# Optimization experiments

Measured on AMD Instinct MI355X. Metric: run time of the kernel, lower is better.

The kernel has to match this reference:

```python
import jax, jax.numpy as jnp
from jax import lax
import numpy as np

B, T, IN = 256, 128, 64
H = 1024            # unified hidden size (encoder fc/lstm == decoder lstm, required by the code)
QW, QL = 128, 128
V = QW * QL         # decoder_output_size_fc
K, DELTA = 5, 16


def _lin(x, w, b):
    return x @ w.T + b


def _lstm(x, h0, c0, wih, whh, bih, bhh):
    # x: [B,T,I]; h0,c0: [B,H]. PyTorch gate order: i, f, g, o.
    xg = jnp.einsum('bti,gi->btg', x, wih) + bih  # precompute input projections [B,T,4H]
    def step(carry, xt):
        h, c = carry
        g = xt + h @ whh.T + bhh
        i, f, gg, o = jnp.split(g, 4, axis=-1)
        c = jax.nn.sigmoid(f) * c + jax.nn.sigmoid(i) * jnp.tanh(gg)
        h = jax.nn.sigmoid(o) * jnp.tanh(c)
        return (h, c), h
    (h, c), ys = lax.scan(step, (h0, c0), jnp.swapaxes(xg, 0, 1))
    return jnp.swapaxes(ys, 0, 1), h, c


def setup_inputs() -> dict:
    key = jax.random.key(0)
    ks = iter(jax.random.split(key, 64))
    def u(shape, fan):
        s = 1.0 / np.sqrt(fan)
        return jax.random.uniform(next(ks), shape, jnp.float32, -s, s)
    def lin_p(o, i):
        return u((o, i), i), u((o,), i)
    def lstm_p(i, h):
        return u((4 * h, i), h), u((4 * h, h), h), u((4 * h,), h), u((4 * h,), h)
    d = {'x': jax.random.normal(next(ks), (B, T, IN), jnp.float32)}
    d['efc1_w'], d['efc1_b'] = lin_p(H, IN)
    d['efc2_w'], d['efc2_b'] = lin_p(H, H)
    d['efc3_w'], d['efc3_b'] = lin_p(H, H)
    d['el1_wih'], d['el1_whh'], d['el1_bih'], d['el1_bhh'] = lstm_p(H, H)
    d['el2_wih'], d['el2_whh'], d['el2_bih'], d['el2_bhh'] = lstm_p(H, H)
    d['dl1_wih'], d['dl1_whh'], d['dl1_bih'], d['dl1_bhh'] = lstm_p(H, H)
    d['dl2_wih'], d['dl2_whh'], d['dl2_bih'], d['dl2_bhh'] = lstm_p(H, H)
    d['dfc1_w'], d['dfc1_b'] = lin_p(H, H)
    d['dfc2_w'], d['dfc2_b'] = lin_p(H, H)
    d['dfc3_w'], d['dfc3_b'] = lin_p(V, H)
    d['fqw_w'], d['fqw_b'] = lin_p(H // 2, QW)
    d['fql_w'], d['fql_b'] = lin_p(H // 2, QL)
    return d


def _forward(x, efc1_w, efc1_b, efc2_w, efc2_b, efc3_w, efc3_b,
             el1_wih, el1_whh, el1_bih, el1_bhh, el2_wih, el2_whh, el2_bih, el2_bhh,
             dl1_wih, dl1_whh, dl1_bih, dl1_bhh, dl2_wih, dl2_whh, dl2_bih, dl2_bhh,
             dfc1_w, dfc1_b, dfc2_w, dfc2_b, dfc3_w, dfc3_b,
             fqw_w, fqw_b, fql_w, fql_b):
    b = x.shape[0]
    # ---- encoder: 3 plain linears (no activation, as in source), then two stacked LSTMs ----
    e = _lin(_lin(_lin(x, efc1_w, efc1_b), efc2_w, efc2_b), efc3_w, efc3_b)
    z = jnp.zeros((b, H), x.dtype)
    e, h1, c1 = _lstm(e, z, z, el1_wih, el1_whh, el1_bih, el1_bhh)
    e, h2, c2 = _lstm(e, z, z, el2_wih, el2_whh, el2_bih, el2_bhh)  # lstm2 gets fresh zero state, as in source
    xs = e[:, -1:, :]  # last timestep [B,1,H]

    def once(xs, h1, c1, h2, c2):
        xs, h1, c1 = _lstm(xs, h1, c1, dl1_wih, dl1_whh, dl1_bih, dl1_bhh)
        xs, h2, c2 = _lstm(xs, h2, c2, dl2_wih, dl2_whh, dl2_bih, dl2_bhh)
        xs = _lin(_lin(_lin(xs, dfc1_w, dfc1_b), dfc2_w, dfc2_b), dfc3_w, dfc3_b)
        return xs, h1, c1, h2, c2

    def beam(scores, kcur, decoded, step):
        # scores: [B,V]; top-k == torch.sort(descending)[:, :kcur]
        _, idx = lax.top_k(scores, kcur)
        fw = idx // QL  # find_w
        fl = idx % QL   # find_l
        iw = jax.nn.one_hot(fw, QW, dtype=scores.dtype)  # [B,kcur,QW]
        il = jax.nn.one_hot(fl, QL, dtype=scores.dtype)  # [B,kcur,QL]
        decoded = decoded.at[:, step, :kcur, 0].set(fl.astype(decoded.dtype))
        decoded = decoded.at[:, step, :kcur, 1].set(fw.astype(decoded.dtype))
        return iw, il, decoded

    out, h1, c1, h2, c2 = once(xs, h1, c1, h2, c2)
    decoded = jnp.zeros((b, DELTA, K, 2), jnp.float32)
    iw, il, decoded = beam(out[:, 0, :], K, decoded, 0)
    iw = _lin(iw, fqw_w, fqw_b)  # [B,K,H/2]
    il = _lin(il, fql_w, fql_b)
    # source sets decoder_K = 1 after the first step: only beam slot 0 is ever expanded
    for t in range(DELTA - 1):
        emb = jnp.concatenate([iw[:, 0, :], il[:, 0, :]], axis=-1)[:, None, :]  # [B,1,H]
        out, h1, c1, h2, c2 = once(emb, h1, c1, h2, c2)
        iw, il, decoded = beam(out[:, 0, :], 1, decoded, t + 1)
        iw = _lin(iw, fqw_w, fqw_b)
        il = _lin(il, fql_w, fql_b)
    return decoded


def reference(x, efc1_w, efc1_b, efc2_w, efc2_b, efc3_w, efc3_b,
              el1_wih, el1_whh, el1_bih, el1_bhh, el2_wih, el2_whh, el2_bih, el2_bhh,
              dl1_wih, dl1_whh, dl1_bih, dl1_bhh, dl2_wih, dl2_whh, dl2_bih, dl2_bhh,
              dfc1_w, dfc1_b, dfc2_w, dfc2_b, dfc3_w, dfc3_b,
              fqw_w, fqw_b, fql_w, fql_b):
    return _forward(x, efc1_w, efc1_b, efc2_w, efc2_b, efc3_w, efc3_b,
                    el1_wih, el1_whh, el1_bih, el1_bhh, el2_wih, el2_whh, el2_bih, el2_bhh,
                    dl1_wih, dl1_whh, dl1_bih, dl1_bhh, dl2_wih, dl2_whh, dl2_bih, dl2_bhh,
                    dfc1_w, dfc1_b, dfc2_w, dfc2_b, dfc3_w, dfc3_b,
                    fqw_w, fqw_b, fql_w, fql_b)
```

## Files before the change

### kernel.cpp

```cpp
#include <hip/hip_runtime.h>
#include <math.h>

#define Hn     1024
#define Bn     256
#define Tn     128
#define Vn     16384
#define DELTAn 16
#define Kn     5
#define QLn    128

typedef _Float16 h8 __attribute__((ext_vector_type(8)));
typedef _Float16 h4 __attribute__((ext_vector_type(4)));
typedef float    f32x4 __attribute__((ext_vector_type(4)));

#define MFMA16(a, b, c) __builtin_amdgcn_mfma_f32_16x16x32_f16(a, b, c, 0, 0, 0)

#define WFRAG_4096 8388608

__global__ __launch_bounds__(256) void wconv_frag(
    const float* __restrict__ W, _Float16* __restrict__ wf, int ngb)
{
    int wid  = (blockIdx.x * 256 + threadIdx.x) >> 6;
    int lane = threadIdx.x & 63;
    int gb = wid >> 5, ks = wid & 31;
    if (gb >= ngb) return;
    const float* src = W + (size_t)(gb * 16 + (lane & 15)) * 1024 + ks * 32 + (lane >> 4) * 8;
    float4 v0 = *(const float4*)src;
    float4 v1 = *(const float4*)(src + 4);
    float vv[8] = {v0.x, v0.y, v0.z, v0.w, v1.x, v1.y, v1.z, v1.w};
    h8 vh, vl;
    #pragma unroll
    for (int j = 0; j < 8; ++j) {
        _Float16 hh = (_Float16)vv[j];
        vh[j] = hh;
        vl[j] = (_Float16)(vv[j] - (float)hh);
    }
    _Float16* dst = wf + ((size_t)(gb * 32 + ks) * 2) * 512 + lane * 8;
    *(h8*)dst        = vh;
    *(h8*)(dst + 512) = vl;
}

__global__ __launch_bounds__(256) void gemm_nt_128(
    const float* __restrict__ A, int lda, const float* __restrict__ W, int K,
    const float* __restrict__ bias, _Float16* __restrict__ yhi,
    _Float16* __restrict__ ylo, int ldy)
{
    __shared__ float As[16 * 132];
    __shared__ float Bs[16 * 132];
    const int bm   = blockIdx.y << 7;
    const int bn   = blockIdx.x << 7;
    const int tid  = threadIdx.x;
    const int tx   = (tid & 15) << 3;
    const int ty   = (tid >> 4) << 3;
    const int lrow = tid >> 1;
    const int lk   = (tid & 1) << 3;

    float acc[8][8] = {};
    const float* arow = A + (size_t)(bm + lrow) * lda + lk;
    const float* brow = W + (size_t)(bn + lrow) * K   + lk;

    for (int kt = 0; kt < K; kt += 16) {
        float4 a0 = *(const float4*)(arow + kt);
        float4 a1 = *(const float4*)(arow + kt + 4);
        float4 b0 = *(const float4*)(brow + kt);
        float4 b1 = *(const float4*)(brow + kt + 4);
        __syncthreads();
        As[(lk + 0) * 132 + lrow] = a0.x; As[(lk + 1) * 132 + lrow] = a0.y;
        As[(lk + 2) * 132 + lrow] = a0.z; As[(lk + 3) * 132 + lrow] = a0.w;
        As[(lk + 4) * 132 + lrow] = a1.x; As[(lk + 5) * 132 + lrow] = a1.y;
        As[(lk + 6) * 132 + lrow] = a1.z; As[(lk + 7) * 132 + lrow] = a1.w;
        Bs[(lk + 0) * 132 + lrow] = b0.x; Bs[(lk + 1) * 132 + lrow] = b0.y;
        Bs[(lk + 2) * 132 + lrow] = b0.z; Bs[(lk + 3) * 132 + lrow] = b0.w;
        Bs[(lk + 4) * 132 + lrow] = b1.x; Bs[(lk + 5) * 132 + lrow] = b1.y;
        Bs[(lk + 6) * 132 + lrow] = b1.z; Bs[(lk + 7) * 132 + lrow] = b1.w;
        __syncthreads();
        #pragma unroll
        for (int k = 0; k < 16; ++k) {
            float4 x0 = *(const float4*)(As + k * 132 + ty);
            float4 x1 = *(const float4*)(As + k * 132 + ty + 4);
            float4 y0 = *(const float4*)(Bs + k * 132 + tx);
            float4 y1 = *(const float4*)(Bs + k * 132 + tx + 4);
            float av[8] = {x0.x, x0.y, x0.z, x0.w, x1.x, x1.y, x1.z, x1.w};
            float bv[8] = {y0.x, y0.y, y0.z, y0.w, y1.x, y1.y, y1.z, y1.w};
            #pragma unroll
            for (int i = 0; i < 8; ++i)
                #pragma unroll
                for (int j = 0; j < 8; ++j)
                    acc[i][j] += av[i] * bv[j];
        }
    }

    #pragma unroll
    for (int i = 0; i < 8; ++i) {
        h8 vh, vl;
        #pragma unroll
        for (int j = 0; j < 8; ++j) {
            float v = acc[i][j] + bias[bn + tx + j];
            _Float16 hh = (_Float16)v;
            vh[j] = hh;
            vl[j] = (_Float16)(v - (float)hh);
        }
        size_t ro = (size_t)(bm + ty + i) * ldy + bn + tx;
        *(h8*)(yhi + ro) = vh;
        *(h8*)(ylo + ro) = vl;
    }
}

__global__ __launch_bounds__(256) void gemm_mfma4(
    const _Float16* __restrict__ Ahi, const _Float16* __restrict__ Alo, long long lda,
    const _Float16* __restrict__ wf, const float* __restrict__ bias,
    float* __restrict__ Y, long long ldy,
    _Float16* __restrict__ yhi, _Float16* __restrict__ ylo, int log2mt)
{
    __shared__ _Float16 lds[2][256 * 40];
    const int lin  = blockIdx.x;
    const int bt   = (lin >> 3) & ((1 << log2mt) - 1);
    const int nt   = (lin & 7) | ((lin >> (3 + log2mt)) << 3);
    const int bn   = nt << 6;
    const int bmB  = bt << 8;
    const int tid  = threadIdx.x;
    const int lane = tid & 63, wv = tid >> 6;
    const int l15  = lane & 15, quad = lane >> 4;
    const int r    = tid;

    f32x4 acc[4][4];
    #pragma unroll
    for (int mi = 0; mi < 4; ++mi)
        #pragma unroll
        for (int nf = 0; nf < 4; ++nf) acc[mi][nf] = (f32x4){0.f, 0.f, 0.f, 0.f};

    h8 ph[4], pl[4];
    h8 BhA[4], BlA[4], BhB[4], BlB[4];
    {
        size_t off = (size_t)(bmB + r) * lda;
        #pragma unroll
        for (int j = 0; j < 4; ++j) {
            ph[j] = *(const h8*)(Ahi + off + j * 8);
            pl[j] = *(const h8*)(Alo + off + j * 8);
        }
        #pragma unroll
        for (int nf = 0; nf < 4; ++nf) {
            const _Float16* bp = wf + ((size_t)(((nt << 2) + nf) * 32) * 2) * 512 + lane * 8;
            BhA[nf] = *(const h8*)bp;
            BlA[nf] = *(const h8*)(bp + 512);
        }
    }

#define G4_SI(SI, BHU, BLU, BHF, BLF)                                          \
    {                                                                          \
        __syncthreads();                                                       \
        _Pragma("unroll")                                                      \
        for (int j = 0; j < 4; ++j) {                                          \
            *(h8*)(&lds[0][r * 40 + j * 8]) = ph[j];                           \
            *(h8*)(&lds[1][r * 40 + j * 8]) = pl[j];                           \
        }                                                                      \
        __syncthreads();                                                       \
        {                                                                      \
            int sn = ((SI) + 1 < 32) ? (SI) + 1 : (SI);                        \
            size_t off = (size_t)(bmB + r) * lda + (sn << 5);                  \
            _Pragma("unroll")                                                  \
            for (int j = 0; j < 4; ++j) {                                      \
                ph[j] = *(const h8*)(Ahi + off + j * 8);                       \
                pl[j] = *(const h8*)(Alo + off + j * 8);                       \
            }                                                                  \
            _Pragma("unroll")                                                  \
            for (int nf = 0; nf < 4; ++nf) {                                   \
                const _Float16* bp = wf +                                      \
                    ((size_t)(((nt << 2) + nf) * 32 + sn) * 2) * 512 + lane * 8;\
                BHF[nf] = *(const h8*)bp;                                      \
                BLF[nf] = *(const h8*)(bp + 512);                              \
            }                                                                  \
        }                                                                      \
        h8 axh[4], axl[4];                                                     \
        _Pragma("unroll")                                                      \
        for (int mi = 0; mi < 4; ++mi) {                                       \
            int row = (wv << 6) + (mi << 4) + l15;                             \
            axh[mi] = *(const h8*)(&lds[0][row * 40 + quad * 8]);              \
            axl[mi] = *(const h8*)(&lds[1][row * 40 + quad * 8]);              \
        }                                                                      \
        _Pragma("unroll")                                                      \
        for (int nf = 0; nf < 4; ++nf)                                         \
            _Pragma("unroll")                                                  \
            for (int mi = 0; mi < 4; ++mi) {                                   \
                acc[mi][nf] = MFMA16(axh[mi], BHU[nf], acc[mi][nf]);           \
                acc[mi][nf] = MFMA16(axh[mi], BLU[nf], acc[mi][nf]);           \
                acc[mi][nf] = MFMA16(axl[mi], BHU[nf], acc[mi][nf]);           \
            }                                                                  \
    }

    for (int si = 0; si < 32; si += 2) {
        G4_SI(si,     BhA, BlA, BhB, BlB);
        G4_SI(si + 1, BhB, BlB, BhA, BlA);
    }
#undef G4_SI

    #pragma unroll
    for (int nf = 0; nf < 4; ++nf) {
        int col = bn + nf * 16 + l15;
        float bv = bias[col];
        #pragma unroll
        for (int mi = 0; mi < 4; ++mi) {
            #pragma unroll
            for (int rr = 0; rr < 4; ++rr) {
                int m = bmB + (wv << 6) + (mi << 4) + (quad << 2) + rr;
                float v = acc[mi][nf][rr] + bv;
                size_t ro = (size_t)m * ldy + col;
                if (yhi) {
                    _Float16 hh = (_Float16)v;
                    yhi[ro] = hh;
                    ylo[ro] = (_Float16)(v - (float)hh);
                } else {
                    Y[ro] = v;
                }
            }
        }
    }
}

__global__ __launch_bounds__(256, 2) void gemm_mfma_s(
    const _Float16* __restrict__ Ahi, const _Float16* __restrict__ Alo, long long lda,
    const _Float16* __restrict__ wf, const float* __restrict__ bias,
    _Float16* __restrict__ yhi, _Float16* __restrict__ ylo, long long ldy)
{
    __shared__ _Float16 lds[2][64 * 40];
    const int bn   = blockIdx.x << 6;
    const int bm   = blockIdx.y << 6;
    const int tid  = threadIdx.x;
    const int lane = tid & 63, wv = tid >> 6;
    const int l15  = lane & 15, quad = lane >> 4;
    const int r    = tid >> 2, kq = (tid & 3) << 3;

    f32x4 acc[4];
    #pragma unroll
    for (int nf = 0; nf < 4; ++nf) acc[nf] = (f32x4){0.f, 0.f, 0.f, 0.f};

    h8 pAh, pAl;
    h8 BhA[4], BlA[4], BhB[4], BlB[4];
    {
        size_t off = (size_t)(bm + r) * lda + kq;
        pAh = *(const h8*)(Ahi + off);
        pAl = *(const h8*)(Alo + off);
        #pragma unroll
        for (int nf = 0; nf < 4; ++nf) {
            const _Float16* bp = wf + ((size_t)(((bn >> 4) + nf) * 32) * 2) * 512 + lane * 8;
            BhA[nf] = *(const h8*)bp;
            BlA[nf] = *(const h8*)(bp + 512);
        }
    }

#define GS_SI(SI, BHU, BLU, BHF, BLF)                                          \
    {                                                                          \
        __syncthreads();                                                       \
        *(h8*)(&lds[0][r * 40 + kq]) = pAh;                                    \
        *(h8*)(&lds[1][r * 40 + kq]) = pAl;                                    \
        __syncthreads();                                                       \
        {                                                                      \
            int sn = ((SI) + 1 < 32) ? (SI) + 1 : (SI);                        \
            size_t off = (size_t)(bm + r) * lda + (sn << 5) + kq;              \
            pAh = *(const h8*)(Ahi + off);                                     \
            pAl = *(const h8*)(Alo + off);                                     \
            _Pragma("unroll")                                                  \
            for (int nf = 0; nf < 4; ++nf) {                                   \
                const _Float16* bp = wf +                                      \
                    ((size_t)(((bn >> 4) + nf) * 32 + sn) * 2) * 512 + lane * 8;\
                BHF[nf] = *(const h8*)bp;                                      \
                BLF[nf] = *(const h8*)(bp + 512);                              \
            }                                                                  \
        }                                                                      \
        int row = (wv << 4) + l15;                                             \
        h8 axh = *(const h8*)(&lds[0][row * 40 + quad * 8]);                   \
        h8 axl = *(const h8*)(&lds[1][row * 40 + quad * 8]);                   \
        _Pragma("unroll")                                                      \
        for (int nf = 0; nf < 4; ++nf) {                                       \
            acc[nf] = MFMA16(axh, BHU[nf], acc[nf]);                           \
            acc[nf] = MFMA16(axh, BLU[nf], acc[nf]);                           \
            acc[nf] = MFMA16(axl, BHU[nf], acc[nf]);                           \
        }                                                                      \
    }

    for (int si = 0; si < 32; si += 2) {
        GS_SI(si,     BhA, BlA, BhB, BlB);
        GS_SI(si + 1, BhB, BlB, BhA, BlA);
    }
#undef GS_SI

    #pragma unroll
    for (int nf = 0; nf < 4; ++nf) {
        int col = bn + nf * 16 + l15;
        float bv = bias[col];
        #pragma unroll
        for (int rr = 0; rr < 4; ++rr) {
            int m = bm + (wv << 4) + (quad << 2) + rr;
            float v = acc[nf][rr] + bv;
            size_t ro = (size_t)m * ldy + col;
            _Float16 hh = (_Float16)v;
            yhi[ro] = hh;
            ylo[ro] = (_Float16)(v - (float)hh);
        }
    }
}

struct LstmSet {
    const _Float16 *xhi, *xlo; long long ldx;
    const _Float16 *hphi, *hplo;
    const _Float16 *wf;
    const float *bih, *bhh;
    float *c;
    _Float16 *hohi, *holo;
};

__global__ __launch_bounds__(256, 2) void lstm_mfma4(LstmSet s0, LstmSet s1)
{
    const int lin = blockIdx.x;
    const int bt  = (lin >> 3) & 3;
    const int jz  = (lin & 7) | ((lin >> 5) << 3);
    const int jt  = jz & 63;
    LstmSet s = (jz >> 6) ? s1 : s0;
    if (s.wf == nullptr) return;
    __shared__ _Float16 lds[2][64 * 72];
    const int tid  = threadIdx.x;
    const int bm   = bt << 6;
    const int lane = tid & 63, wv = tid >> 6;
    const int l15  = lane & 15, quad = lane >> 4;
    const int r    = tid >> 2, kq = (tid & 3) << 4;

    f32x4 acc[4];
    #pragma unroll
    for (int nf = 0; nf < 4; ++nf) acc[nf] = (f32x4){0.f, 0.f, 0.f, 0.f};

    h8 pA[4];
    h8 BhA[8], BlA[8], BhB[8], BlB[8];
    {
        size_t off = (size_t)(bm + r) * s.ldx + kq;
        pA[0] = *(const h8*)(s.xhi + off); pA[1] = *(const h8*)(s.xhi + off + 8);
        pA[2] = *(const h8*)(s.xlo + off); pA[3] = *(const h8*)(s.xlo + off + 8);
        #pragma unroll
        for (int sub = 0; sub < 2; ++sub)
            #pragma unroll
            for (int nf = 0; nf < 4; ++nf) {
                const _Float16* bp = s.wf +
                    ((size_t)((nf * 64 + jt) * 32 + sub) * 2) * 512 + lane * 8;
                BhA[sub * 4 + nf] = *(const h8*)bp;
                BlA[sub * 4 + nf] = *(const h8*)(bp + 512);
            }
    }

#define LS_SI(SI, BHU, BLU, BHF, BLF)                                          \
    {                                                                          \
        __syncthreads();                                                       \
        *(h8*)(&lds[0][r * 72 + kq])     = pA[0];                              \
        *(h8*)(&lds[0][r * 72 + kq + 8]) = pA[1];                              \
        *(h8*)(&lds[1][r * 72 + kq])     = pA[2];                              \
        *(h8*)(&lds[1][r * 72 + kq + 8]) = pA[3];                              \
        __syncthreads();                                                       \
        {                                                                      \
            int sn  = ((SI) + 1 < 32) ? (SI) + 1 : (SI);                       \
            int phx = sn >> 4;                                                 \
            const _Float16* xh = phx ? s.hphi : s.xhi;                         \
            const _Float16* xl = phx ? s.hplo : s.xlo;                         \
            long long ld = phx ? Hn : s.ldx;                                   \
            size_t off = (size_t)(bm + r) * ld + ((sn & 15) << 6) + kq;        \
            pA[0] = *(const h8*)(xh + off); pA[1] = *(const h8*)(xh + off + 8);\
            pA[2] = *(const h8*)(xl + off); pA[3] = *(const h8*)(xl + off + 8);\
            const _Float16* wb = s.wf + (size_t)(sn >> 4) * WFRAG_4096;        \
            int ksb = (sn & 15) << 1;                                          \
            _Pragma("unroll")                                                  \
            for (int sub = 0; sub < 2; ++sub)                                  \
                _Pragma("unroll")                                              \
                for (int nf = 0; nf < 4; ++nf) {                               \
                    const _Float16* bp = wb +                                  \
                        ((size_t)((nf * 64 + jt) * 32 + ksb + sub) * 2) * 512  \
                        + lane * 8;                                            \
                    BHF[sub * 4 + nf] = *(const h8*)bp;                        \
                    BLF[sub * 4 + nf] = *(const h8*)(bp + 512);                \
                }                                                              \
        }                                                                      \
        const _Float16* wbc = s.wf + (size_t)((SI) >> 4) * WFRAG_4096;         \
        (void)wbc;                                                             \
        _Pragma("unroll")                                                      \
        for (int sub = 0; sub < 2; ++sub) {                                    \
            int row = (wv << 4) + l15;                                         \
            h8 axh = *(const h8*)(&lds[0][row * 72 + sub * 32 + quad * 8]);    \
            h8 axl = *(const h8*)(&lds[1][row * 72 + sub * 32 + quad * 8]);    \
            _Pragma("unroll")                                                  \
            for (int nf = 0; nf < 4; ++nf) {                                   \
                acc[nf] = MFMA16(axh, BHU[sub * 4 + nf], acc[nf]);             \
                acc[nf] = MFMA16(axh, BLU[sub * 4 + nf], acc[nf]);             \
                acc[nf] = MFMA16(axl, BHU[sub * 4 + nf], acc[nf]);             \
            }                                                                  \
        }                                                                      \
    }

    for (int si = 0; si < 32; si += 2) {
        LS_SI(si,     BhA, BlA, BhB, BlB);
        LS_SI(si + 1, BhB, BlB, BhA, BlA);
    }
#undef LS_SI

    float bs[4];
    #pragma unroll
    for (int nf = 0; nf < 4; ++nf) {
        int br = nf * Hn + (jt << 4) + l15;
        bs[nf] = s.bih[br] + s.bhh[br];
    }
    #pragma unroll
    for (int rr = 0; rr < 4; ++rr) {
        int m = (wv << 4) + (quad << 2) + rr;
        size_t idx = (size_t)(bm + m) * Hn + (jt << 4) + l15;
        float gi = acc[0][rr] + bs[0];
        float gf = acc[1][rr] + bs[1];
        float gg = acc[2][rr] + bs[2];
        float go = acc[3][rr] + bs[3];
        float cv = s.c[idx];
        float si_ = 1.0f / (1.0f + expf(-gi));
        float sf  = 1.0f / (1.0f + expf(-gf));
        float so  = 1.0f / (1.0f + expf(-go));
        float cn = sf * cv + si_ * tanhf(gg);
        float hn = so * tanhf(cn);
        s.c[idx] = cn;
        _Float16 hh = (_Float16)hn;
        s.hohi[idx] = hh;
        s.holo[idx] = (_Float16)(hn - (float)hh);
    }
}

__global__ __launch_bounds__(256) void beam_kernel(
    const float* __restrict__ scores, float* __restrict__ decoded,
    _Float16* __restrict__ embhi, _Float16* __restrict__ emblo,
    const float* __restrict__ fqw_w, const float* __restrict__ fqw_b,
    const float* __restrict__ fql_w, const float* __restrict__ fql_b,
    int step, int kcur)
{
    __shared__ float svals[256];
    __shared__ int   sidx[256];
    __shared__ int   sel[Kn];
    const int b   = blockIdx.x;
    const int tid = threadIdx.x;
    const float* row = scores + (size_t)b * Vn;

    for (int rr = 0; rr < kcur; ++rr) {
        float best = -INFINITY;
        int   bidx = Vn;
        for (int i = tid; i < Vn; i += 256) {
            bool skip = false;
            for (int q = 0; q < rr; ++q) if (sel[q] == i) skip = true;
            float v = row[i];
            if (!skip && v > best) { best = v; bidx = i; }
        }
        svals[tid] = best; sidx[tid] = bidx;
        __syncthreads();
        for (int s = 128; s > 0; s >>= 1) {
            if (tid < s) {
                float v2 = svals[tid + s]; int i2 = sidx[tid + s];
                if (v2 > svals[tid] || (v2 == svals[tid] && i2 < sidx[tid])) {
                    svals[tid] = v2; sidx[tid] = i2;
                }
            }
            __syncthreads();
        }
        if (tid == 0) sel[rr] = sidx[0];
        __syncthreads();
    }

    if (tid < kcur) {
        int s_ = sel[tid];
        int fw = s_ / QLn, fl = s_ % QLn;
        float* dp = decoded + ((size_t)(b * DELTAn + step) * Kn + tid) * 2;
        dp[0] = (float)fl;
        dp[1] = (float)fw;
    }

    const int fw0 = sel[0] / QLn;
    const int fl0 = sel[0] % QLn;
    for (int o = tid; o < 512; o += 256) {
        float v0 = fqw_w[o * QLn + fw0] + fqw_b[o];
        float v1 = fql_w[o * QLn + fl0] + fql_b[o];
        _Float16 h0 = (_Float16)v0;
        _Float16 h1 = (_Float16)v1;
        size_t i0 = (size_t)b * Hn + o;
        embhi[i0]       = h0; emblo[i0]       = (_Float16)(v0 - (float)h0);
        embhi[i0 + 512] = h1; emblo[i0 + 512] = (_Float16)(v1 - (float)h1);
    }
}

extern "C" void kernel_launch(void* const* d_in, const int* in_sizes, int n_in,
                              void* d_out, int out_size, void* d_ws, size_t ws_size,
                              hipStream_t stream)
{
    int ii = 0;
    const float* x       = (const float*)d_in[ii++];
    const float* efc1_w  = (const float*)d_in[ii++];
    const float* efc1_b  = (const float*)d_in[ii++];
    const float* efc2_w  = (const float*)d_in[ii++];
    const float* efc2_b  = (const float*)d_in[ii++];
    const float* efc3_w  = (const float*)d_in[ii++];
    const float* efc3_b  = (const float*)d_in[ii++];
    const float* el1_wih = (const float*)d_in[ii++];
    const float* el1_whh = (const float*)d_in[ii++];
    const float* el1_bih = (const float*)d_in[ii++];
    const float* el1_bhh = (const float*)d_in[ii++];
    const float* el2_wih = (const float*)d_in[ii++];
    const float* el2_whh = (const float*)d_in[ii++];
    const float* el2_bih = (const float*)d_in[ii++];
    const float* el2_bhh = (const float*)d_in[ii++];
    const float* dl1_wih = (const float*)d_in[ii++];
    const float* dl1_whh = (const float*)d_in[ii++];
    const float* dl1_bih = (const float*)d_in[ii++];
    const float* dl1_bhh = (const float*)d_in[ii++];
    const float* dl2_wih = (const float*)d_in[ii++];
    const float* dl2_whh = (const float*)d_in[ii++];
    const float* dl2_bih = (const float*)d_in[ii++];
    const float* dl2_bhh = (const float*)d_in[ii++];
    const float* dfc1_w  = (const float*)d_in[ii++];
    const float* dfc1_b  = (const float*)d_in[ii++];
    const float* dfc2_w  = (const float*)d_in[ii++];
    const float* dfc2_b  = (const float*)d_in[ii++];
    const float* dfc3_w  = (const float*)d_in[ii++];
    const float* dfc3_b  = (const float*)d_in[ii++];
    const float* fqw_w   = (const float*)d_in[ii++];
    const float* fqw_b   = (const float*)d_in[ii++];
    const float* fql_w   = (const float*)d_in[ii++];
    const float* fql_b   = (const float*)d_in[ii++];

    float* out = (float*)d_out;

    char* p = (char*)d_ws;
    auto alloc = [&](size_t bytes) { char* q = p; p += (bytes + 255) & ~(size_t)255; return q; };
    _Float16* bufhi = (_Float16*)alloc((size_t)32768 * 1024 * 2);
    _Float16* buflo = (_Float16*)alloc((size_t)32768 * 1024 * 2);
    _Float16* slot0 = (_Float16*)alloc((size_t)2 * WFRAG_4096 * 2);
    _Float16* slot1 = (_Float16*)alloc((size_t)2 * WFRAG_4096 * 2);
    _Float16* efw2  = (_Float16*)alloc((size_t)2097152 * 2);
    _Float16* efw3  = (_Float16*)alloc((size_t)2097152 * 2);
    _Float16* dfw1  = (_Float16*)alloc((size_t)2097152 * 2);
    _Float16* dfw2  = (_Float16*)alloc((size_t)2097152 * 2);
    float*    scores= (float*)alloc((size_t)256 * Vn * 4);
    char*  zbase = p;
    float* c1    = (float*)alloc((size_t)256 * Hn * 4);
    float* c2    = (float*)alloc((size_t)256 * Hn * 4);
    _Float16* h1hiA = (_Float16*)alloc((size_t)256 * Hn * 2);
    _Float16* h1loA = (_Float16*)alloc((size_t)256 * Hn * 2);
    _Float16* h2hiA = (_Float16*)alloc((size_t)256 * Hn * 2);
    _Float16* h2loA = (_Float16*)alloc((size_t)256 * Hn * 2);
    size_t zbytes = (size_t)(p - zbase);
    _Float16* h1hiB = (_Float16*)alloc((size_t)256 * Hn * 2);
    _Float16* h1loB = (_Float16*)alloc((size_t)256 * Hn * 2);
    _Float16* h2hiB = (_Float16*)alloc((size_t)256 * Hn * 2);
    _Float16* h2loB = (_Float16*)alloc((size_t)256 * Hn * 2);
    _Float16* f1hi  = (_Float16*)alloc((size_t)256 * Hn * 2);
    _Float16* f1lo  = (_Float16*)alloc((size_t)256 * Hn * 2);
    _Float16* f2hi  = (_Float16*)alloc((size_t)256 * Hn * 2);
    _Float16* f2lo  = (_Float16*)alloc((size_t)256 * Hn * 2);
    _Float16* embhi = (_Float16*)alloc((size_t)256 * Hn * 2);
    _Float16* emblo = (_Float16*)alloc((size_t)256 * Hn * 2);

    _Float16* t1hi = (_Float16*)scores;
    _Float16* t1lo = t1hi + (size_t)4096 * 1024;
    _Float16* t2hi = slot0;
    _Float16* t2lo = t2hi + (size_t)4096 * 1024;
    _Float16* dfc3f = bufhi;

    const long long TH = (long long)Tn * Hn;

    hipLaunchKernelGGL(wconv_frag, dim3(512), dim3(256), 0, stream, efc2_w, efw2, 64);
    hipLaunchKernelGGL(wconv_frag, dim3(512), dim3(256), 0, stream, efc3_w, efw3, 64);

    for (int c = 0; c < 8; ++c) {
        const float* xc = x + (size_t)c * 4096 * 64;
        size_t ofs = (size_t)c * 4096 * 1024;
        hipLaunchKernelGGL(gemm_nt_128, dim3(8, 32), dim3(256), 0, stream,
                           xc, 64, efc1_w, 64, efc1_b, t1hi, t1lo, Hn);
        hipLaunchKernelGGL(gemm_mfma4, dim3(256), dim3(256), 0, stream,
                           t1hi, t1lo, (long long)Hn, efw2, efc2_b,
                           (float*)nullptr, (long long)Hn, t2hi, t2lo, 4);
        hipLaunchKernelGGL(gemm_mfma4, dim3(256), dim3(256), 0, stream,
                           t2hi, t2lo, (long long)Hn, efw3, efc3_b,
                           (float*)nullptr, (long long)Hn, bufhi + ofs, buflo + ofs, 4);
    }

    hipLaunchKernelGGL(wconv_frag, dim3(2048), dim3(256), 0, stream, el1_wih, slot0, 256);
    hipLaunchKernelGGL(wconv_frag, dim3(2048), dim3(256), 0, stream, el1_whh, slot0 + WFRAG_4096, 256);
    hipLaunchKernelGGL(wconv_frag, dim3(2048), dim3(256), 0, stream, el2_wih, slot1, 256);
    hipLaunchKernelGGL(wconv_frag, dim3(2048), dim3(256), 0, stream, el2_whh, slot1 + WFRAG_4096, 256);

    hipMemsetAsync(zbase, 0, zbytes, stream);

    _Float16 *h1hiC = h1hiA, *h1loC = h1loA, *h1hiN = h1hiB, *h1loN = h1loB;
    _Float16 *h2hiC = h2hiA, *h2loC = h2loA, *h2hiN = h2hiB, *h2loN = h2loB;
    _Float16* tp;
    for (int d = 0; d <= Tn; ++d) {
        LstmSet s0 = {}, s1 = {};
        if (d < Tn) {
            s0.xhi = bufhi + (size_t)d * Hn; s0.xlo = buflo + (size_t)d * Hn; s0.ldx = TH;
            s0.hphi = h1hiC; s0.hplo = h1loC; s0.wf = slot0;
            s0.bih = el1_bih; s0.bhh = el1_bhh; s0.c = c1;
            s0.hohi = h1hiN; s0.holo = h1loN;
        }
        if (d >= 1) {
            s1.xhi = h1hiC; s1.xlo = h1loC; s1.ldx = Hn;
            s1.hphi = h2hiC; s1.hplo = h2loC; s1.wf = slot1;
            s1.bih = el2_bih; s1.bhh = el2_bhh; s1.c = c2;
            s1.hohi = h2hiN; s1.holo = h2loN;
        }
        hipLaunchKernelGGL(lstm_mfma4, dim3(512), dim3(256), 0, stream, s0, s1);
        if (d < Tn)  { tp = h1hiC; h1hiC = h1hiN; h1hiN = tp;
                       tp = h1loC; h1loC = h1loN; h1loN = tp; }
        if (d >= 1)  { tp = h2hiC; h2hiC = h2hiN; h2hiN = tp;
                       tp = h2loC; h2loC = h2loN; h2loN = tp; }
    }

    hipLaunchKernelGGL(wconv_frag, dim3(2048), dim3(256), 0, stream, dl1_wih, slot0, 256);
    hipLaunchKernelGGL(wconv_frag, dim3(2048), dim3(256), 0, stream, dl1_whh, slot0 + WFRAG_4096, 256);
    hipLaunchKernelGGL(wconv_frag, dim3(2048), dim3(256), 0, stream, dl2_wih, slot1, 256);
    hipLaunchKernelGGL(wconv_frag, dim3(2048), dim3(256), 0, stream, dl2_whh, slot1 + WFRAG_4096, 256);
    hipLaunchKernelGGL(wconv_frag, dim3(8192), dim3(256), 0, stream, dfc3_w, dfc3f, 1024);
    hipLaunchKernelGGL(wconv_frag, dim3(512), dim3(256), 0, stream, dfc1_w, dfw1, 64);
    hipLaunchKernelGGL(wconv_frag, dim3(512), dim3(256), 0, stream, dfc2_w, dfw2, 64);

    hipMemsetAsync(out, 0, (size_t)out_size * sizeof(float), stream);

    for (int it = 0; it < DELTAn; ++it) {
        LstmSet s0 = {}, sx = {};
        s0.xhi = (it == 0) ? h2hiC : embhi;
        s0.xlo = (it == 0) ? h2loC : emblo;
        s0.ldx = Hn;
        s0.hphi = h1hiC; s0.hplo = h1loC; s0.wf = slot0;
        s0.bih = dl1_bih; s0.bhh = dl1_bhh; s0.c = c1;
        s0.hohi = h1hiN; s0.holo = h1loN;
        hipLaunchKernelGGL(lstm_mfma4, dim3(256), dim3(256), 0, stream, s0, sx);
        tp = h1hiC; h1hiC = h1hiN; h1hiN = tp;
        tp = h1loC; h1loC = h1loN; h1loN = tp;

        LstmSet s2 = {};
        s2.xhi = h1hiC; s2.xlo = h1loC; s2.ldx = Hn;
        s2.hphi = h2hiC; s2.hplo = h2loC; s2.wf = slot1;
        s2.bih = dl2_bih; s2.bhh = dl2_bhh; s2.c = c2;
        s2.hohi = h2hiN; s2.holo = h2loN;
        hipLaunchKernelGGL(lstm_mfma4, dim3(256), dim3(256), 0, stream, s2, sx);
        tp = h2hiC; h2hiC = h2hiN; h2hiN = tp;
        tp = h2loC; h2loC = h2loN; h2loN = tp;

        hipLaunchKernelGGL(gemm_mfma_s, dim3(16, 4), dim3(256), 0, stream,
                           h2hiC, h2loC, (long long)Hn, dfw1, dfc1_b,
                           f1hi, f1lo, (long long)Hn);
        hipLaunchKernelGGL(gemm_mfma_s, dim3(16, 4), dim3(256), 0, stream,
                           f1hi, f1lo, (long long)Hn, dfw2, dfc2_b,
                           f2hi, f2lo, (long long)Hn);
        hipLaunchKernelGGL(gemm_mfma4, dim3(256), dim3(256), 0, stream,
                           f2hi, f2lo, (long long)Hn, dfc3f, dfc3_b,
                           scores, (long long)Vn, (_Float16*)nullptr, (_Float16*)nullptr, 0);
        hipLaunchKernelGGL(beam_kernel, dim3(Bn), dim3(256), 0, stream,
                           scores, out, embhi, emblo, fqw_w, fqw_b, fql_w, fql_b,
                           it, (it == 0) ? Kn : 1);
    }
}
```

Before: 10.88 ms.

## Use 128x128 MFMA tiles for LSTM steps and FC GEMMs

Result: slower. 13.42 ms (+23.3%).

```diff
diff --git a/kernel.cpp b/kernel.cpp
--- a/kernel.cpp
+++ b/kernel.cpp
@@ -106,117 +106,6 @@
     }
 }
 
-__global__ __launch_bounds__(256) void gemm_mfma4(
-    const _Float16* __restrict__ Ahi, const _Float16* __restrict__ Alo, long long lda,
-    const _Float16* __restrict__ wf, const float* __restrict__ bias,
-    float* __restrict__ Y, long long ldy,
-    _Float16* __restrict__ yhi, _Float16* __restrict__ ylo, int log2mt)
-{
-    __shared__ _Float16 lds[2][256 * 40];
-    const int lin  = blockIdx.x;
-    const int bt   = (lin >> 3) & ((1 << log2mt) - 1);
-    const int nt   = (lin & 7) | ((lin >> (3 + log2mt)) << 3);
-    const int bn   = nt << 6;
-    const int bmB  = bt << 8;
-    const int tid  = threadIdx.x;
-    const int lane = tid & 63, wv = tid >> 6;
-    const int l15  = lane & 15, quad = lane >> 4;
-    const int r    = tid;
-
-    f32x4 acc[4][4];
-    #pragma unroll
-    for (int mi = 0; mi < 4; ++mi)
-        #pragma unroll
-        for (int nf = 0; nf < 4; ++nf) acc[mi][nf] = (f32x4){0.f, 0.f, 0.f, 0.f};
-
-    h8 ph[4], pl[4];
-    h8 BhA[4], BlA[4], BhB[4], BlB[4];
-    {
-        size_t off = (size_t)(bmB + r) * lda;
-        #pragma unroll
-        for (int j = 0; j < 4; ++j) {
-            ph[j] = *(const h8*)(Ahi + off + j * 8);
-            pl[j] = *(const h8*)(Alo + off + j * 8);
-        }
-        #pragma unroll
-        for (int nf = 0; nf < 4; ++nf) {
-            const _Float16* bp = wf + ((size_t)(((nt << 2) + nf) * 32) * 2) * 512 + lane * 8;
-            BhA[nf] = *(const h8*)bp;
-            BlA[nf] = *(const h8*)(bp + 512);
-        }
-    }
-
-#define G4_SI(SI, BHU, BLU, BHF, BLF)                                          \
-    {                                                                          \
-        __syncthreads();                                                       \
-        _Pragma("unroll")                                                      \
-        for (int j = 0; j < 4; ++j) {                                          \
-            *(h8*)(&lds[0][r * 40 + j * 8]) = ph[j];                           \
-            *(h8*)(&lds[1][r * 40 + j * 8]) = pl[j];                           \
-        }                                                                      \
-        __syncthreads();                                                       \
-        {                                                                      \
-            int sn = ((SI) + 1 < 32) ? (SI) + 1 : (SI);                        \
-            size_t off = (size_t)(bmB + r) * lda + (sn << 5);                  \
-            _Pragma("unroll")                                                  \
-            for (int j = 0; j < 4; ++j) {                                      \
-                ph[j] = *(const h8*)(Ahi + off + j * 8);                       \
-                pl[j] = *(const h8*)(Alo + off + j * 8);                       \
-            }                                                                  \
-            _Pragma("unroll")                                                  \
-            for (int nf = 0; nf < 4; ++nf) {                                   \
-                const _Float16* bp = wf +                                      \
-                    ((size_t)(((nt << 2) + nf) * 32 + sn) * 2) * 512 + lane * 8;\
-                BHF[nf] = *(const h8*)bp;                                      \
-                BLF[nf] = *(const h8*)(bp + 512);                              \
-            }                                                                  \
-        }                                                                      \
-        h8 axh[4], axl[4];                                                     \
-        _Pragma("unroll")                                                      \
-        for (int mi = 0; mi < 4; ++mi) {                                       \
-            int row = (wv << 6) + (mi << 4) + l15;                             \
-            axh[mi] = *(const h8*)(&lds[0][row * 40 + quad * 8]);              \
-            axl[mi] = *(const h8*)(&lds[1][row * 40 + quad * 8]);              \
-        }                                                                      \
-        _Pragma("unroll")                                                      \
-        for (int nf = 0; nf < 4; ++nf)                                         \
-            _Pragma("unroll")                                                  \
-            for (int mi = 0; mi < 4; ++mi) {                                   \
-                acc[mi][nf] = MFMA16(axh[mi], BHU[nf], acc[mi][nf]);           \
-                acc[mi][nf] = MFMA16(axh[mi], BLU[nf], acc[mi][nf]);           \
-                acc[mi][nf] = MFMA16(axl[mi], BHU[nf], acc[mi][nf]);           \
-            }                                                                  \
-    }
-
-    for (int si = 0; si < 32; si += 2) {
-        G4_SI(si,     BhA, BlA, BhB, BlB);
-        G4_SI(si + 1, BhB, BlB, BhA, BlA);
-    }
-#undef G4_SI
-
-    #pragma unroll
-    for (int nf = 0; nf < 4; ++nf) {
-        int col = bn + nf * 16 + l15;
-        float bv = bias[col];
-        #pragma unroll
-        for (int mi = 0; mi < 4; ++mi) {
-            #pragma unroll
-            for (int rr = 0; rr < 4; ++rr) {
-                int m = bmB + (wv << 6) + (mi << 4) + (quad << 2) + rr;
-                float v = acc[mi][nf][rr] + bv;
-                size_t ro = (size_t)m * ldy + col;
-                if (yhi) {
-                    _Float16 hh = (_Float16)v;
-                    yhi[ro] = hh;
-                    ylo[ro] = (_Float16)(v - (float)hh);
-                } else {
-                    Y[ro] = v;
-                }
-            }
-        }
-    }
-}
-
 __global__ __launch_bounds__(256, 2) void gemm_mfma_s(
     const _Float16* __restrict__ Ahi, const _Float16* __restrict__ Alo, long long lda,
     const _Float16* __restrict__ wf, const float* __restrict__ bias,
@@ -300,6 +189,124 @@
     }
 }
 
+__global__ __launch_bounds__(256, 1) void mm128_fc(
+    const _Float16* __restrict__ Ahi, const _Float16* __restrict__ Alo, long long lda,
+    const _Float16* __restrict__ wf, const float* __restrict__ bias,
+    float* __restrict__ Y, long long ldy,
+    _Float16* __restrict__ yhi, _Float16* __restrict__ ylo)
+{
+    __shared__ _Float16 lds[2][128 * 72];
+    const int bn   = blockIdx.x << 7;
+    const int bm   = blockIdx.y << 7;
+    const int tid  = threadIdx.x;
+    const int lane = tid & 63, wv = tid >> 6;
+    const int wm   = wv >> 1, wn = wv & 1;
+    const int l15  = lane & 15, quad = lane >> 4;
+    const int r    = tid >> 1, kh = (tid & 1) << 5;
+    const int gbb  = (bn >> 4) + (wn << 2);
+
+    f32x4 acc[4][4];
+    #pragma unroll
+    for (int mi = 0; mi < 4; ++mi)
+        #pragma unroll
+        for (int nf = 0; nf < 4; ++nf) acc[mi][nf] = (f32x4){0.f, 0.f, 0.f, 0.f};
+
+    h8 pA[8];
+    h8 BhA[8], BlA[8], BhB[8], BlB[8];
+    {
+        size_t off = (size_t)(bm + r) * lda + kh;
+        #pragma unroll
+        for (int j = 0; j < 4; ++j) {
+            pA[j]     = *(const h8*)(Ahi + off + j * 8);
+            pA[4 + j] = *(const h8*)(Alo + off + j * 8);
+        }
+        #pragma unroll
+        for (int s = 0; s < 2; ++s)
+            #pragma unroll
+            for (int nf = 0; nf < 4; ++nf) {
+                const _Float16* bp = wf + ((size_t)((gbb + nf) * 32 + s) * 2) * 512 + lane * 8;
+                BhA[s * 4 + nf] = *(const h8*)bp;
+                BlA[s * 4 + nf] = *(const h8*)(bp + 512);
+            }
+    }
+
+#define F_SI(SI, BHU, BLU, BHF, BLF)                                           \
+    {                                                                          \
+        __syncthreads();                                                       \
+        _Pragma("unroll")                                                      \
+        for (int j = 0; j < 4; ++j) {                                          \
+            *(h8*)(&lds[0][r * 72 + kh + j * 8]) = pA[j];                      \
+            *(h8*)(&lds[1][r * 72 + kh + j * 8]) = pA[4 + j];                  \
+        }                                                                      \
+        __syncthreads();                                                       \
+        {                                                                      \
+            int sn = ((SI) + 1 < 16) ? (SI) + 1 : (SI);                        \
+            size_t off = (size_t)(bm + r) * lda + (sn << 6) + kh;              \
+            _Pragma("unroll")                                                  \
+            for (int j = 0; j < 4; ++j) {                                      \
+                pA[j]     = *(const h8*)(Ahi + off + j * 8);                   \
+                pA[4 + j] = *(const h8*)(Alo + off + j * 8);                   \
+            }                                                                  \
+            int ksb = sn << 1;                                                 \
+            _Pragma("unroll")                                                  \
+            for (int s = 0; s < 2; ++s)                                        \
+                _Pragma("unroll")                                              \
+                for (int nf = 0; nf < 4; ++nf) {                               \
+                    const _Float16* bp = wf +                                  \
+                        ((size_t)((gbb + nf) * 32 + ksb + s) * 2) * 512 + lane * 8; \
+                    BHF[s * 4 + nf] = *(const h8*)bp;                          \
+                    BLF[s * 4 + nf] = *(const h8*)(bp + 512);                  \
+                }                                                              \
+        }                                                                      \
+        _Pragma("unroll")                                                      \
+        for (int s = 0; s < 2; ++s) {                                          \
+            h8 axh[4], axl[4];                                                 \
+            _Pragma("unroll")                                                  \
+            for (int mi = 0; mi < 4; ++mi) {                                   \
+                int row = (wm << 6) + (mi << 4) + l15;                         \
+                axh[mi] = *(const h8*)(&lds[0][row * 72 + s * 32 + quad * 8]); \
+                axl[mi] = *(const h8*)(&lds[1][row * 72 + s * 32 + quad * 8]); \
+            }                                                                  \
+            _Pragma("unroll")                                                  \
+            for (int nf = 0; nf < 4; ++nf)                                     \
+                _Pragma("unroll")                                              \
+                for (int mi = 0; mi < 4; ++mi) {                               \
+                    acc[mi][nf] = MFMA16(axh[mi], BHU[s * 4 + nf], acc[mi][nf]); \
+                    acc[mi][nf] = MFMA16(axh[mi], BLU[s * 4 + nf], acc[mi][nf]); \
+                    acc[mi][nf] = MFMA16(axl[mi], BHU[s * 4 + nf], acc[mi][nf]); \
+                }                                                              \
+        }                                                                      \
+    }
+
+    for (int si = 0; si < 16; si += 2) {
+        F_SI(si,     BhA, BlA, BhB, BlB);
+        F_SI(si + 1, BhB, BlB, BhA, BlA);
+    }
+#undef F_SI
+
+    #pragma unroll
+    for (int nf = 0; nf < 4; ++nf) {
+        int col = bn + (wn << 6) + (nf << 4) + l15;
+        float bv = bias[col];
+        #pragma unroll
+        for (int mi = 0; mi < 4; ++mi) {
+            #pragma unroll
+            for (int rr = 0; rr < 4; ++rr) {
+                int m = bm + (wm << 6) + (mi << 4) + (quad << 2) + rr;
+                float v = acc[mi][nf][rr] + bv;
+                size_t ro = (size_t)m * ldy + col;
+                if (yhi) {
+                    _Float16 hh = (_Float16)v;
+                    yhi[ro] = hh;
+                    ylo[ro] = (_Float16)(v - (float)hh);
+                } else {
+                    Y[ro] = v;
+                }
+            }
+        }
+    }
+}
+
 struct LstmSet {
     const _Float16 *xhi, *xlo; long long ldx;
     const _Float16 *hphi, *hplo;
@@ -309,49 +316,56 @@
     _Float16 *hohi, *holo;
 };
 
-__global__ __launch_bounds__(256, 2) void lstm_mfma4(LstmSet s0, LstmSet s1)
+__global__ __launch_bounds__(256, 1) void lstm_mfma5(LstmSet s0, LstmSet s1)
 {
     const int lin = blockIdx.x;
-    const int bt  = (lin >> 3) & 3;
-    const int jz  = (lin & 7) | ((lin >> 5) << 3);
-    const int jt  = jz & 63;
-    LstmSet s = (jz >> 6) ? s1 : s0;
+    const int jt  = (lin & 7) | (((lin >> 4) & 3) << 3);
+    const int bt  = (lin >> 3) & 1;
+    LstmSet s = (lin >> 6) ? s1 : s0;
     if (s.wf == nullptr) return;
-    __shared__ _Float16 lds[2][64 * 72];
+    __shared__ _Float16 lds[2][128 * 72];
     const int tid  = threadIdx.x;
-    const int bm   = bt << 6;
+    const int bm   = bt << 7;
     const int lane = tid & 63, wv = tid >> 6;
+    const int wm   = wv >> 1, wn = wv & 1;
     const int l15  = lane & 15, quad = lane >> 4;
-    const int r    = tid >> 2, kq = (tid & 3) << 4;
-
-    f32x4 acc[4];
-    #pragma unroll
-    for (int nf = 0; nf < 4; ++nf) acc[nf] = (f32x4){0.f, 0.f, 0.f, 0.f};
-
-    h8 pA[4];
+    const int r    = tid >> 1, kh = (tid & 1) << 5;
+    const int jg   = (jt << 1) + wn;
+
+    f32x4 acc[4][4];
+    #pragma unroll
+    for (int mi = 0; mi < 4; ++mi)
+        #pragma unroll
+        for (int nf = 0; nf < 4; ++nf) acc[mi][nf] = (f32x4){0.f, 0.f, 0.f, 0.f};
+
+    h8 pA[8];
     h8 BhA[8], BlA[8], BhB[8], BlB[8];
     {
-        size_t off = (size_t)(bm + r) * s.ldx + kq;
-        pA[0] = *(const h8*)(s.xhi + off); pA[1] = *(const h8*)(s.xhi + off + 8);
-        pA[2] = *(const h8*)(s.xlo + off); pA[3] = *(const h8*)(s.xlo + off + 8);
-        #pragma unroll
-        for (int sub = 0; sub < 2; ++sub)
+        size_t off = (size_t)(bm + r) * s.ldx + kh;
+        #pragma unroll
+        for (int j = 0; j < 4; ++j) {
+            pA[j]     = *(const h8*)(s.xhi + off + j * 8);
+            pA[4 + j] = *(const h8*)(s.xlo + off + j * 8);
+        }
+        #pragma unroll
+        for (int ss = 0; ss < 2; ++ss)
             #pragma unroll
             for (int nf = 0; nf < 4; ++nf) {
                 const _Float16* bp = s.wf +
-                    ((size_t)((nf * 64 + jt) * 32 + sub) * 2) * 512 + lane * 8;
-                BhA[sub * 4 + nf] = *(const h8*)bp;
-                BlA[sub * 4 + nf] = *(const h8*)(bp + 512);
+                    ((size_t)((nf * 64 + jg) * 32 + ss) * 2) * 512 + lane * 8;
+                BhA[ss * 4 + nf] = *(const h8*)bp;
+                BlA[ss * 4 + nf] = *(const h8*)(bp + 512);
             }
     }
 
-#define LS_SI(SI, BHU, BLU, BHF, BLF)                                          \
+#define L5_SI(SI, BHU, BLU, BHF, BLF)                                          \
     {                                                                          \
         __syncthreads();                                                       \
-        *(h8*)(&lds[0][r * 72 + kq])     = pA[0];                              \
-        *(h8*)(&lds[0][r * 72 + kq + 8]) = pA[1];                              \
-        *(h8*)(&lds[1][r * 72 + kq])     = pA[2];                              \
-        *(h8*)(&lds[1][r * 72 + kq + 8]) = pA[3];                              \
+        _Pragma("unroll")                                                      \
+        for (int j = 0; j < 4; ++j) {                                          \
+            *(h8*)(&lds[0][r * 72 + kh + j * 8]) = pA[j];                      \
+            *(h8*)(&lds[1][r * 72 + kh + j * 8]) = pA[4 + j];                  \
+        }                                                                      \
         __syncthreads();                                                       \
         {                                                                      \
             int sn  = ((SI) + 1 < 32) ? (SI) + 1 : (SI);                       \
@@ -359,68 +373,78 @@
             const _Float16* xh = phx ? s.hphi : s.xhi;                         \
             const _Float16* xl = phx ? s.hplo : s.xlo;                         \
             long long ld = phx ? Hn : s.ldx;                                   \
-            size_t off = (size_t)(bm + r) * ld + ((sn & 15) << 6) + kq;        \
-            pA[0] = *(const h8*)(xh + off); pA[1] = *(const h8*)(xh + off + 8);\
-            pA[2] = *(const h8*)(xl + off); pA[3] = *(const h8*)(xl + off + 8);\
+            size_t off = (size_t)(bm + r) * ld + ((sn & 15) << 6) + kh;        \
+            _Pragma("unroll")                                                  \
+            for (int j = 0; j < 4; ++j) {                                      \
+                pA[j]     = *(const h8*)(xh + off + j * 8);                    \
+                pA[4 + j] = *(const h8*)(xl + off + j * 8);                    \
+            }                                                                  \
             const _Float16* wb = s.wf + (size_t)(sn >> 4) * WFRAG_4096;        \
             int ksb = (sn & 15) << 1;                                          \
             _Pragma("unroll")                                                  \
-            for (int sub = 0; sub < 2; ++sub)                                  \
+            for (int ss = 0; ss < 2; ++ss)                                     \
                 _Pragma("unroll")                                              \
                 for (int nf = 0; nf < 4; ++nf) {                               \
                     const _Float16* bp = wb +                                  \
-                        ((size_t)((nf * 64 + jt) * 32 + ksb + sub) * 2) * 512  \
+                        ((size_t)((nf * 64 + jg) * 32 + ksb + ss) * 2) * 512   \
                         + lane * 8;                                            \
-                    BHF[sub * 4 + nf] = *(const h8*)bp;                        \
-                    BLF[sub * 4 + nf] = *(const h8*)(bp + 512);                \
+                    BHF[ss * 4 + nf] = *(const h8*)bp;                         \
+                    BLF[ss * 4 + nf] = *(const h8*)(bp + 512);                 \
                 }                                                              \
         }                                                                      \
-        const _Float16* wbc = s.wf + (size_t)((SI) >> 4) * WFRAG_4096;         \
-        (void)wbc;                                                             \
         _Pragma("unroll")                                                      \
-        for (int sub = 0; sub < 2; ++sub) {                                    \
-            int row = (wv << 4) + l15;                                         \
-            h8 axh = *(const h8*)(&lds[0][row * 72 + sub * 32 + quad * 8]);    \
-            h8 axl = *(const h8*)(&lds[1][row * 72 + sub * 32 + quad * 8]);    \
-            _Pragma("unroll")                                                  \
-            for (int nf = 0; nf < 4; ++nf) {                                   \
-                acc[nf] = MFMA16(axh, BHU[sub * 4 + nf], acc[nf]);             \
-                acc[nf] = MFMA16(axh, BLU[sub * 4 + nf], acc[nf]);             \
-                acc[nf] = MFMA16(axl, BHU[sub * 4 + nf], acc[nf]);             \
+        for (int ss = 0; ss < 2; ++ss) {                                       \
+            h8 axh[4], axl[4];                                                 \
+            _Pragma("unroll")                                                  \
+            for (int mi = 0; mi < 4; ++mi) {                                   \
+                int row = (wm << 6) + (mi << 4) + l15;                         \
+                axh[mi] = *(const h8*)(&lds[0][row * 72 + ss * 32 + quad * 8]);\
+                axl[mi] = *(const h8*)(&lds[1][row * 72 + ss * 32 + quad * 8]);\
             }                                                                  \
+            _Pragma("unroll")                                                  \
+            for (int nf = 0; nf < 4; ++nf)                                     \
+                _Pragma("unroll")                                              \
+                for (int mi = 0; mi < 4; ++mi) {                               \
+                    acc[mi][nf] = MFMA16(axh[mi], BHU[ss * 4 + nf], acc[mi][nf]); \
+                    acc[mi][nf] = MFMA16(axh[mi], BLU[ss * 4 + nf], acc[mi][nf]); \
+                    acc[mi][nf] = MFMA16(axl[mi], BHU[ss * 4 + nf], acc[mi][nf]); \
+                }                                                              \
         }                                                                      \
     }
 
     for (int si = 0; si < 32; si += 2) {
-        LS_SI(si,     BhA, BlA, BhB, BlB);
-        LS_SI(si + 1, BhB, BlB, BhA, BlA);
-    }
-#undef LS_SI
+        L5_SI(si,     BhA, BlA, BhB, BlB);
+        L5_SI(si + 1, BhB, BlB, BhA, BlA);
+    }
+#undef L5_SI
 
     float bs[4];
     #pragma unroll
     for (int nf = 0; nf < 4; ++nf) {
-        int br = nf * Hn + (jt << 4) + l15;
+        int br = nf * Hn + (jg << 4) + l15;
         bs[nf] = s.bih[br] + s.bhh[br];
     }
     #pragma unroll
-    for (int rr = 0; rr < 4; ++rr) {
-        int m = (wv << 4) + (quad << 2) + rr;
-        size_t idx = (size_t)(bm + m) * Hn + (jt << 4) + l15;
-        float gi = acc[0][rr] + bs[0];
-        float gf = acc[1][rr] + bs[1];
-        float gg = acc[2][rr] + bs[2];
-        float go = acc[3][rr] + bs[3];
-        float cv = s.c[idx];
-        float si_ = 1.0f / (1.0f + expf(-gi));
-        float sf  = 1.0f / (1.0f + expf(-gf));
-        float so  = 1.0f / (1.0f + expf(-go));
-        float cn = sf * cv + si_ * tanhf(gg);
-        float hn = so * tanhf(cn);
-        s.c[idx] = cn;
-        _Float16 hh = (_Float16)hn;
-        s.hohi[idx] = hh;
-        s.holo[idx] = (_Float16)(hn - (float)hh);
+    for (int mi = 0; mi < 4; ++mi) {
+        #pragma unroll
+        for (int rr = 0; rr < 4; ++rr) {
+            int m = (wm << 6) + (mi << 4) + (quad << 2) + rr;
+            size_t idx = (size_t)(bm + m) * Hn + (jg << 4) + l15;
+            float gi = acc[mi][0][rr] + bs[0];
+            float gf = acc[mi][1][rr] + bs[1];
+            float gg = acc[mi][2][rr] + bs[2];
+            float go = acc[mi][3][rr] + bs[3];
+            float cv = s.c[idx];
+            float si_ = 1.0f / (1.0f + expf(-gi));
+            float sf  = 1.0f / (1.0f + expf(-gf));
+            float so  = 1.0f / (1.0f + expf(-go));
+            float cn = sf * cv + si_ * tanhf(gg);
+            float hn = so * tanhf(cn);
+            s.c[idx] = cn;
+            _Float16 hh = (_Float16)hn;
+            s.hohi[idx] = hh;
+            s.holo[idx] = (_Float16)(hn - (float)hh);
+        }
     }
 }
 
@@ -570,12 +594,12 @@
         size_t ofs = (size_t)c * 4096 * 1024;
         hipLaunchKernelGGL(gemm_nt_128, dim3(8, 32), dim3(256), 0, stream,
                            xc, 64, efc1_w, 64, efc1_b, t1hi, t1lo, Hn);
-        hipLaunchKernelGGL(gemm_mfma4, dim3(256), dim3(256), 0, stream,
+        hipLaunchKernelGGL(mm128_fc, dim3(8, 32), dim3(256), 0, stream,
                            t1hi, t1lo, (long long)Hn, efw2, efc2_b,
-                           (float*)nullptr, (long long)Hn, t2hi, t2lo, 4);
-        hipLaunchKernelGGL(gemm_mfma4, dim3(256), dim3(256), 0, stream,
+                           (float*)nullptr, (long long)Hn, t2hi, t2lo);
+        hipLaunchKernelGGL(mm128_fc, dim3(8, 32), dim3(256), 0, stream,
                            t2hi, t2lo, (long long)Hn, efw3, efc3_b,
-                           (float*)nullptr, (long long)Hn, bufhi + ofs, buflo + ofs, 4);
+                           (float*)nullptr, (long long)Hn, bufhi + ofs, buflo + ofs);
     }
 
     hipLaunchKernelGGL(wconv_frag, dim3(2048), dim3(256), 0, stream, el1_wih, slot0, 256);
@@ -602,7 +626,7 @@
             s1.bih = el2_bih; s1.bhh = el2_bhh; s1.c = c2;
             s1.hohi = h2hiN; s1.holo = h2loN;
         }
-        hipLaunchKernelGGL(lstm_mfma4, dim3(512), dim3(256), 0, stream, s0, s1);
+        hipLaunchKernelGGL(lstm_mfma5, dim3(128), dim3(256), 0, stream, s0, s1);
         if (d < Tn)  { tp = h1hiC; h1hiC = h1hiN; h1hiN = tp;
                        tp = h1loC; h1loC = h1loN; h1loN = tp; }
         if (d >= 1)  { tp = h2hiC; h2hiC = h2hiN; h2hiN = tp;
@@ -627,7 +651,7 @@
         s0.hphi = h1hiC; s0.hplo = h1loC; s0.wf = slot0;
         s0.bih = dl1_bih; s0.bhh = dl1_bhh; s0.c = c1;
         s0.hohi = h1hiN; s0.holo = h1loN;
-        hipLaunchKernelGGL(lstm_mfma4, dim3(256), dim3(256), 0, stream, s0, sx);
+        hipLaunchKernelGGL(lstm_mfma5, dim3(64), dim3(256), 0, stream, s0, sx);
         tp = h1hiC; h1hiC = h1hiN; h1hiN = tp;
         tp = h1loC; h1loC = h1loN; h1loN = tp;
 
@@ -636,7 +660,7 @@
         s2.hphi = h2hiC; s2.hplo = h2loC; s2.wf = slot1;
         s2.bih = dl2_bih; s2.bhh = dl2_bhh; s2.c = c2;
         s2.hohi = h2hiN; s2.holo = h2loN;
-        hipLaunchKernelGGL(lstm_mfma4, dim3(256), dim3(256), 0, stream, s2, sx);
+        hipLaunchKernelGGL(lstm_mfma5, dim3(64), dim3(256), 0, stream, s2, sx);
         tp = h2hiC; h2hiC = h2hiN; h2hiN = tp;
         tp = h2loC; h2loC = h2loN; h2loN = tp;
 
@@ -646,9 +670,9 @@
         hipLaunchKernelGGL(gemm_mfma_s, dim3(16, 4), dim3(256), 0, stream,
                            f1hi, f1lo, (long long)Hn, dfw2, dfc2_b,
                            f2hi, f2lo, (long long)Hn);
-        hipLaunchKernelGGL(gemm_mfma4, dim3(256), dim3(256), 0, stream,
+        hipLaunchKernelGGL(mm128_fc, dim3(128, 2), dim3(256), 0, stream,
                            f2hi, f2lo, (long long)Hn, dfc3f, dfc3_b,
-                           scores, (long long)Vn, (_Float16*)nullptr, (_Float16*)nullptr, 0);
+                           scores, (long long)Vn, (_Float16*)nullptr, (_Float16*)nullptr);
         hipLaunchKernelGGL(beam_kernel, dim3(Bn), dim3(256), 0, stream,
                            scores, out, embhi, emblo, fqw_w, fqw_b, fql_w, fql_b,
                            it, (it == 0) ? Kn : 1);
```
